# Kernel optimization log

Hardware: AMD Instinct MI355X
Metric: run time of the kernel (lower is better)

The kernel has to match this reference:

```python
import jax, jax.numpy as jnp
import numpy as np
from math import sqrt

D_MODEL = 1024
D_HEAD = 128
TAU = 30.0
B, L = 8, 2048


def setup_inputs() -> dict:
    key = jax.random.key(0)
    k1, k2, k3, k4 = jax.random.split(key, 4)
    x = jax.random.normal(k1, (B, L, D_MODEL), dtype=jnp.float32)
    attention_mask = jnp.ones((B, L), dtype=jnp.int32)
    W_Q = jax.random.normal(k2, (D_HEAD, D_MODEL), dtype=jnp.float32)
    W_K = jax.random.normal(k3, (D_HEAD, D_MODEL), dtype=jnp.float32)
    W_V = jax.random.normal(k4, (D_HEAD, D_MODEL), dtype=jnp.float32)
    return {"input": x, "attention_mask": attention_mask, "W_Q": W_Q, "W_K": W_K, "W_V": W_V}


def reference(input, attention_mask, W_Q, W_K, W_V):
    # Single-head projections: [B, L, d_head]
    Q = input @ W_Q.T
    K = input @ W_K.T
    V = input @ W_V.T
    # Scaled scores: [B, L, L]
    S = jnp.einsum("bqd,bkd->bqk", Q, K) / sqrt(D_HEAD)
    # tanh soft-capping (mode == 'tanh-clipped')
    S = TAU * jnp.tanh(S)
    l = input.shape[1]
    # causal mask: strictly upper triangle -> -inf
    causal = jnp.triu(jnp.ones((l, l), dtype=bool), k=1)
    S = jnp.where(causal[None, :, :], -jnp.inf, S)
    # padding mask on keys: [B, 1, L]
    S = jnp.where(attention_mask[:, None, :] == 0, -jnp.inf, S)
    Attn = jax.nn.softmax(S, axis=-1)
    return Attn @ V
```

## Files before the change

### kernel.cpp

```cpp
#include <hip/hip_runtime.h>
#include <hip/hip_bf16.h>

#define BATCH  8
#define SEQ    2048
#define DMODEL 1024
#define DHEAD  128

typedef __attribute__((ext_vector_type(4))) float f32x4;
typedef __attribute__((ext_vector_type(4))) float f4;
typedef _Float16 f16;
typedef __attribute__((ext_vector_type(8))) _Float16 f16x8;
typedef __attribute__((ext_vector_type(8))) __bf16 bf16x8;
typedef __attribute__((ext_vector_type(16))) unsigned short u16x16;

__device__ __forceinline__ unsigned short f2bf(float f) {
    unsigned u = __builtin_bit_cast(unsigned, f);
    u += 0x7fffu + ((u >> 16) & 1u);
    return (unsigned short)(u >> 16);
}

#if __has_builtin(__builtin_amdgcn_exp2f)
#define EXP2(x) __builtin_amdgcn_exp2f(x)
#else
#define EXP2(x) exp2f(x)
#endif

__device__ __forceinline__ float fast_rcp(float x) {
#if __has_builtin(__builtin_amdgcn_rcpf)
    return __builtin_amdgcn_rcpf(x);
#else
    return 1.0f / x;
#endif
}

__device__ __forceinline__ void async_copy16(const void* g, void* l) {
    __builtin_amdgcn_global_load_lds(
        (const __attribute__((address_space(1))) unsigned int*)g,
        (__attribute__((address_space(3))) unsigned int*)l,
        16, 0, 0);
}

__global__ __launch_bounds__(256) void wsplit_kernel(
    const float* __restrict__ WQ, const float* __restrict__ WK,
    const float* __restrict__ WV, f16* __restrict__ Wsp)
{
    const int gid = blockIdx.x * 256 + threadIdx.x;
    const int row = gid & 127;
    const int hi  = (gid >> 7) & 3;
    const int ks  = (gid >> 9) & 31;
    const int mat = gid >> 14;
    const float* W = (mat < 2) ? WQ : (mat < 4) ? WK : WV;
    const float* src = W + (size_t)row * DMODEL + ks * 32 + hi * 8;
    f4 v0 = *(const f4*)src, v1 = *(const f4*)(src + 4);
    const bool lopart = (mat == 1 || mat == 3);
    f16x8 o;
    #pragma unroll
    for (int j = 0; j < 4; ++j) {
        f16 h0 = (f16)v0[j], h1 = (f16)v1[j];
        o[j]     = lopart ? (f16)(v0[j] - (float)h0) : h0;
        o[j + 4] = lopart ? (f16)(v1[j] - (float)h1) : h1;
    }
    *reinterpret_cast<f16x8*>(Wsp + (size_t)gid * 8) = o;
}

__global__ __launch_bounds__(256) void proj_kernel(
    const float* __restrict__ x, const f16* __restrict__ Wsp,
    f16* __restrict__ Qh, f16* __restrict__ Ql,
    f16* __restrict__ Kh, f16* __restrict__ Kl,
    unsigned short* __restrict__ Vtb)
{
    __shared__ f16 Wl[2][5][4][64][8];
    __shared__ f16 Ax[2][2][4][4][17][8];

    const int tid  = threadIdx.x;
    const int lane = tid & 63;
    const int w    = tid >> 6;
    const int lo   = lane & 15;
    const int hi   = lane >> 4;
    const int m0   = blockIdx.x * 64;
    const int bn   = blockIdx.y;

    const int xrow = tid >> 2;
    const int xg   = tid & 3;
    const int xrb  = xrow >> 4, xro = xrow & 15;

    f32x4 accQ[4] = {}, accK[4] = {}, accV[4] = {};

    const float* xbase = x + (size_t)(m0 + xrow) * DMODEL + xg * 8;
    const f16*   wsrc0 = Wsp + (size_t)(w * 128 + bn * 64 + lane) * 8;

    f4 rx0, rx1;
    auto loadX = [&](int ks) {
        rx0 = *(const f4*)(xbase + ks * 32);
        rx1 = *(const f4*)(xbase + ks * 32 + 4);
    };
    auto writeX = [&](int buf) {
        f16x8 h8, l8;
        #pragma unroll
        for (int j = 0; j < 4; ++j) {
            f16 h0 = (f16)rx0[j]; h8[j]     = h0; l8[j]     = (f16)(rx0[j] - (float)h0);
            f16 h1 = (f16)rx1[j]; h8[j + 4] = h1; l8[j + 4] = (f16)(rx1[j] - (float)h1);
        }
        *reinterpret_cast<f16x8*>(&Ax[buf][0][xrb][xg][xro][0]) = h8;
        *reinterpret_cast<f16x8*>(&Ax[buf][1][xrb][xg][xro][0]) = l8;
    };
    auto stageW = [&](int ks, int buf) {
        #pragma unroll
        for (int m = 0; m < 5; ++m)
            async_copy16(wsrc0 + (size_t)(m * 32 + ks) * 4096,
                         &Wl[buf][m][w][0][0]);
    };

    stageW(0, 0);
    loadX(0);
    writeX(0);
    __syncthreads();

    for (int ks = 0; ks < 32; ++ks) {
        const int cur = ks & 1;
        if (ks < 31) { stageW(ks + 1, cur ^ 1); loadX(ks + 1); }

        f16x8 W5[5];
        #pragma unroll
        for (int m = 0; m < 5; ++m)
            W5[m] = *reinterpret_cast<const f16x8*>(&Wl[cur][m][hi][w * 16 + lo][0]);

        #pragma unroll
        for (int rb = 0; rb < 4; ++rb) {
            f16x8 ah = *reinterpret_cast<const f16x8*>(&Ax[cur][0][rb][hi][lo][0]);
            f16x8 al = *reinterpret_cast<const f16x8*>(&Ax[cur][1][rb][hi][lo][0]);
            accQ[rb] = __builtin_amdgcn_mfma_f32_16x16x32_f16(ah, W5[0], accQ[rb], 0, 0, 0);
            accQ[rb] = __builtin_amdgcn_mfma_f32_16x16x32_f16(ah, W5[1], accQ[rb], 0, 0, 0);
            accQ[rb] = __builtin_amdgcn_mfma_f32_16x16x32_f16(al, W5[0], accQ[rb], 0, 0, 0);
            accK[rb] = __builtin_amdgcn_mfma_f32_16x16x32_f16(ah, W5[2], accK[rb], 0, 0, 0);
            accK[rb] = __builtin_amdgcn_mfma_f32_16x16x32_f16(ah, W5[3], accK[rb], 0, 0, 0);
            accK[rb] = __builtin_amdgcn_mfma_f32_16x16x32_f16(al, W5[2], accK[rb], 0, 0, 0);
            accV[rb] = __builtin_amdgcn_mfma_f32_16x16x32_f16(ah, W5[4], accV[rb], 0, 0, 0);
        }
        if (ks < 31) writeX(cur ^ 1);
        __syncthreads();
    }

    #pragma unroll
    for (int rb = 0; rb < 4; ++rb)
        #pragma unroll
        for (int r = 0; r < 4; ++r) {
            const int m = m0 + rb * 16 + hi * 4 + r;
            const int n = bn * 64 + w * 16 + lo;
            const size_t idx = (size_t)m * DHEAD + n;
            float vq = accQ[rb][r];
            f16 hq = (f16)vq;
            Qh[idx] = hq; Ql[idx] = (f16)(vq - (float)hq);
            float vk = accK[rb][r];
            f16 hk = (f16)vk;
            Kh[idx] = hk; Kl[idx] = (f16)(vk - (float)hk);
            const int bb = m >> 11, l = m & 2047;
            Vtb[((size_t)bb * DHEAD + n) * SEQ + l] = f2bf(accV[rb][r]);
        }
}

#define PART_STRIDE 8256
__global__ __launch_bounds__(512) void attn_kernel(
    const f16* __restrict__ Qh, const f16* __restrict__ Ql,
    const f16* __restrict__ Kh, const f16* __restrict__ Kl,
    const unsigned short* __restrict__ Vtb, const int* __restrict__ mask,
    float* __restrict__ part)
{
    __shared__ f16 Khs[2][64][136];
    __shared__ f16 Kls[2][64][136];
    __shared__ unsigned short Vs[2][128][72];
    __shared__ int Ms[2][64];
    __shared__ unsigned short Plds[8][16][40];

    const int tid  = threadIdx.x;
    const int lane = tid & 63;
    const int w    = tid >> 6;
    const int lo   = lane & 15;
    const int hi   = lane >> 4;
    const int wq   = w & 3;
    const int wk   = w >> 2;
    const int b    = blockIdx.x;
    const int qs   = 31 - (int)blockIdx.y;
    const int z    = blockIdx.z;
    const int qrow = qs * 64 + wq * 16;

    const float c2p = 0.25506061907448296f;
    const float c1  = -86.561702453337804f;

    f16x8 qh[4], ql[4];
    {
        const size_t off = ((size_t)(b * SEQ + qrow + lo)) * DHEAD + hi * 8;
        #pragma unroll
        for (int c = 0; c < 4; ++c) {
            qh[c] = *reinterpret_cast<const f16x8*>(Qh + off + c * 32);
            ql[c] = *reinterpret_cast<const f16x8*>(Ql + off + c * 32);
        }
    }

    const int krow = tid >> 3;
    const int kcol = (tid & 7) * 16;
    const int vrow = tid >> 2;
    const int vcol = (tid & 3) * 16;

    f16x8  rKh0, rKh1, rKl0, rKl1;
    u16x16 rV;
    int    rM = 0;

    auto load_tile = [&](int kb) {
        const size_t koff = ((size_t)(b * SEQ + kb + krow)) * DHEAD + kcol;
        rKh0 = *reinterpret_cast<const f16x8*>(Kh + koff);
        rKh1 = *reinterpret_cast<const f16x8*>(Kh + koff + 8);
        rKl0 = *reinterpret_cast<const f16x8*>(Kl + koff);
        rKl1 = *reinterpret_cast<const f16x8*>(Kl + koff + 8);
        rV   = *reinterpret_cast<const u16x16*>(Vtb + ((size_t)b * DHEAD + vrow) * SEQ + kb + vcol);
        if (tid < 64) rM = mask[b * SEQ + kb + tid];
    };
    auto write_tile = [&](int buf) {
        *reinterpret_cast<f16x8*>(&Khs[buf][krow][kcol])     = rKh0;
        *reinterpret_cast<f16x8*>(&Khs[buf][krow][kcol + 8]) = rKh1;
        *reinterpret_cast<f16x8*>(&Kls[buf][krow][kcol])     = rKl0;
        *reinterpret_cast<f16x8*>(&Kls[buf][krow][kcol + 8]) = rKl1;
        *reinterpret_cast<u16x16*>(&Vs[buf][vrow][vcol]) = rV;
        if (tid < 64) Ms[buf][tid] = rM;
    };

    load_tile(z * 64);
    write_tile(0);
    __syncthreads();

    f32x4 acc[8] = {};
    float rs[4] = {0.f, 0.f, 0.f, 0.f};

    int cnt = 0;
    for (int it = z; it <= qs; it += 2, ++cnt) {
        const int cur = cnt & 1;
        const bool havenext = (it + 2 <= qs);
        if (havenext) load_tile((it + 2) * 64);

        const int kb = it * 64 + wk * 32;
        if (kb <= qrow + 15) {
            #pragma unroll
            for (int h = 0; h < 2; ++h) {
                f32x4 s = {};
                #pragma unroll
                for (int c = 0; c < 4; ++c) {
                    f16x8 fkh = *reinterpret_cast<const f16x8*>(&Khs[cur][wk * 32 + h * 16 + lo][c * 32 + hi * 8]);
                    f16x8 fkl = *reinterpret_cast<const f16x8*>(&Kls[cur][wk * 32 + h * 16 + lo][c * 32 + hi * 8]);
                    s = __builtin_amdgcn_mfma_f32_16x16x32_f16(qh[c], fkh, s, 0, 0, 0);
                    s = __builtin_amdgcn_mfma_f32_16x16x32_f16(qh[c], fkl, s, 0, 0, 0);
                    s = __builtin_amdgcn_mfma_f32_16x16x32_f16(ql[c], fkh, s, 0, 0, 0);
                }
                const int key = kb + h * 16 + lo;
                const int mk  = Ms[cur][wk * 32 + h * 16 + lo];
                #pragma unroll
                for (int r = 0; r < 4; ++r) {
                    const int q = qrow + hi * 4 + r;
                    float t = EXP2(s[r] * c2p);
                    float p = EXP2(c1 * fast_rcp(t + 1.0f));
                    p = (key <= q && mk != 0) ? p : 0.0f;
                    rs[r] += p;
                    Plds[w][hi * 4 + r][h * 16 + lo] = f2bf(p);
                }
            }
            bf16x8 pa = *reinterpret_cast<const bf16x8*>(&Plds[w][lo][hi * 8]);
            #pragma unroll
            for (int dt = 0; dt < 8; ++dt) {
                bf16x8 vf = *reinterpret_cast<const bf16x8*>(&Vs[cur][dt * 16 + lo][wk * 32 + hi * 8]);
                acc[dt] = __builtin_amdgcn_mfma_f32_16x16x32_bf16(pa, vf, acc[dt], 0, 0, 0);
            }
        }

        if (havenext) write_tile(cur ^ 1);
        __syncthreads();
    }

    float* red = (float*)&Khs[0][0][0];
    if (wk == 1) {
        float* dst = red + ((size_t)wq * 64 + lane) * 36;
        #pragma unroll
        for (int dt = 0; dt < 8; ++dt)
            #pragma unroll
            for (int r = 0; r < 4; ++r) dst[dt * 4 + r] = acc[dt][r];
        #pragma unroll
        for (int r = 0; r < 4; ++r) dst[32 + r] = rs[r];
    }
    __syncthreads();
    if (wk == 0) {
        const float* src = red + ((size_t)wq * 64 + lane) * 36;
        #pragma unroll
        for (int dt = 0; dt < 8; ++dt)
            #pragma unroll
            for (int r = 0; r < 4; ++r) acc[dt][r] += src[dt * 4 + r];
        float rsum[4];
        #pragma unroll
        for (int r = 0; r < 4; ++r) {
            float v = rs[r] + src[32 + r];
            v += __shfl_xor(v, 1);
            v += __shfl_xor(v, 2);
            v += __shfl_xor(v, 4);
            v += __shfl_xor(v, 8);
            rsum[r] = v;
        }
        float* P = part + (((size_t)b * 32 + qs) * 2 + z) * PART_STRIDE;
        #pragma unroll
        for (int dt = 0; dt < 8; ++dt)
            #pragma unroll
            for (int r = 0; r < 4; ++r)
                P[(wq * 16 + hi * 4 + r) * 128 + dt * 16 + lo] = acc[dt][r];
        if (lo == 0)
            #pragma unroll
            for (int r = 0; r < 4; ++r)
                P[8192 + wq * 16 + hi * 4 + r] = rsum[r];
    }
}

__global__ __launch_bounds__(256) void merge_kernel(
    const float* __restrict__ part, float* __restrict__ out)
{
    const int gid = blockIdx.x * 256 + threadIdx.x;
    const int col = (gid & 31) * 4;
    const int q   = gid >> 5;
    const int b   = q >> 11, l = q & 2047;
    const int qs  = l >> 6, row = l & 63;
    const float* P0 = part + (((size_t)b * 32 + qs) * 2) * PART_STRIDE;
    const float* P1 = P0 + PART_STRIDE;
    f4 a0 = *(const f4*)(P0 + row * 128 + col);
    f4 a1 = *(const f4*)(P1 + row * 128 + col);
    float inv = fast_rcp(P0[8192 + row] + P1[8192 + row]);
    f4 o;
    #pragma unroll
    for (int j = 0; j < 4; ++j) o[j] = (a0[j] + a1[j]) * inv;
    *(f4*)(out + (size_t)q * 128 + col) = o;
}

extern "C" void kernel_launch(void* const* d_in, const int* in_sizes, int n_in,
                              void* d_out, int out_size, void* d_ws, size_t ws_size,
                              hipStream_t stream) {
    const float* x   = (const float*)d_in[0];
    const int*   msk = (const int*)d_in[1];
    const float* WQ  = (const float*)d_in[2];
    const float* WK  = (const float*)d_in[3];
    const float* WV  = (const float*)d_in[4];
    float* out = (float*)d_out;

    const size_t NE = (size_t)BATCH * SEQ * DHEAD;
    f16* Qh = (f16*)d_ws;
    f16* Ql = Qh + NE;
    f16* Kh = Ql + NE;
    f16* Kl = Kh + NE;
    unsigned short* Vtb = (unsigned short*)(Kl + NE);
    f16* Wsp = (f16*)(Vtb + NE);
    float* part = (float*)(Wsp + (size_t)5 * 32 * 4096);

    wsplit_kernel<<<320, 256, 0, stream>>>(WQ, WK, WV, Wsp);
    proj_kernel<<<dim3(BATCH * SEQ / 64, 2), 256, 0, stream>>>(x, Wsp, Qh, Ql, Kh, Kl, Vtb);
    attn_kernel<<<dim3(BATCH, 32, 2), 512, 0, stream>>>(Qh, Ql, Kh, Kl, Vtb, msk, part);
    merge_kernel<<<2048, 256, 0, stream>>>(part, out);
}
```

Measured before the change: 98.89 us.

## Load projection weights directly from global and deepen x staging to 128-wide K

The projection kernel no longer stages weight fragments through LDS with async global-to-LDS copies. Each lane now reads its W fragments straight from global memory into registers. The x tile is staged 128 K-elements at a time instead of 32, so there are 8 iterations with 8 barriers instead of 32. Launch bounds now request 2 blocks per SM. The intent is to cut LDS traffic and synchronisation, at the cost of more register pressure and weight loads that depend on cache hits instead of a prefetch.

New measurement: 92.68 us. 1.07x faster.

```diff
diff --git a/kernel.cpp b/kernel.cpp
--- a/kernel.cpp
+++ b/kernel.cpp
@@ -31,13 +31,6 @@
 #else
     return 1.0f / x;
 #endif
-}
-
-__device__ __forceinline__ void async_copy16(const void* g, void* l) {
-    __builtin_amdgcn_global_load_lds(
-        (const __attribute__((address_space(1))) unsigned int*)g,
-        (__attribute__((address_space(3))) unsigned int*)l,
-        16, 0, 0);
 }
 
 __global__ __launch_bounds__(256) void wsplit_kernel(
@@ -63,14 +56,13 @@
     *reinterpret_cast<f16x8*>(Wsp + (size_t)gid * 8) = o;
 }
 
-__global__ __launch_bounds__(256) void proj_kernel(
+__global__ __launch_bounds__(256, 2) void proj_kernel(
     const float* __restrict__ x, const f16* __restrict__ Wsp,
     f16* __restrict__ Qh, f16* __restrict__ Ql,
     f16* __restrict__ Kh, f16* __restrict__ Kl,
     unsigned short* __restrict__ Vtb)
 {
-    __shared__ f16 Wl[2][5][4][64][8];
-    __shared__ f16 Ax[2][2][4][4][17][8];
+    __shared__ f16 Ax[2][2][4][16][17][8];
 
     const int tid  = threadIdx.x;
     const int lane = tid & 63;
@@ -79,6 +71,7 @@
     const int hi   = lane >> 4;
     const int m0   = blockIdx.x * 64;
     const int bn   = blockIdx.y;
+    const int fi   = hi * 128 + bn * 64 + w * 16 + lo;
 
     const int xrow = tid >> 2;
     const int xg   = tid & 3;
@@ -87,57 +80,63 @@
     f32x4 accQ[4] = {}, accK[4] = {}, accV[4] = {};
 
     const float* xbase = x + (size_t)(m0 + xrow) * DMODEL + xg * 8;
-    const f16*   wsrc0 = Wsp + (size_t)(w * 128 + bn * 64 + lane) * 8;
-
-    f4 rx0, rx1;
-    auto loadX = [&](int ks) {
-        rx0 = *(const f4*)(xbase + ks * 32);
-        rx1 = *(const f4*)(xbase + ks * 32 + 4);
+    const f16*   wbase = Wsp + (size_t)fi * 8;
+
+    f4 rx[8];
+    auto loadX = [&](int ks4) {
+        const float* p = xbase + ks4 * 128;
+        #pragma unroll
+        for (int k = 0; k < 4; ++k) {
+            rx[2 * k]     = *(const f4*)(p + k * 32);
+            rx[2 * k + 1] = *(const f4*)(p + k * 32 + 4);
+        }
+    };
+    auto cvt8 = [](f4 v0, f4 v1, f16x8& h8, f16x8& l8) {
+        #pragma unroll
+        for (int j = 0; j < 4; ++j) {
+            f16 h0 = (f16)v0[j]; h8[j]     = h0; l8[j]     = (f16)(v0[j] - (float)h0);
+            f16 h1 = (f16)v1[j]; h8[j + 4] = h1; l8[j + 4] = (f16)(v1[j] - (float)h1);
+        }
     };
     auto writeX = [&](int buf) {
-        f16x8 h8, l8;
-        #pragma unroll
-        for (int j = 0; j < 4; ++j) {
-            f16 h0 = (f16)rx0[j]; h8[j]     = h0; l8[j]     = (f16)(rx0[j] - (float)h0);
-            f16 h1 = (f16)rx1[j]; h8[j + 4] = h1; l8[j + 4] = (f16)(rx1[j] - (float)h1);
-        }
-        *reinterpret_cast<f16x8*>(&Ax[buf][0][xrb][xg][xro][0]) = h8;
-        *reinterpret_cast<f16x8*>(&Ax[buf][1][xrb][xg][xro][0]) = l8;
-    };
-    auto stageW = [&](int ks, int buf) {
-        #pragma unroll
-        for (int m = 0; m < 5; ++m)
-            async_copy16(wsrc0 + (size_t)(m * 32 + ks) * 4096,
-                         &Wl[buf][m][w][0][0]);
-    };
-
-    stageW(0, 0);
+        #pragma unroll
+        for (int k = 0; k < 4; ++k) {
+            f16x8 h8, l8;
+            cvt8(rx[2 * k], rx[2 * k + 1], h8, l8);
+            *reinterpret_cast<f16x8*>(&Ax[buf][0][xrb][xg + 4 * k][xro][0]) = h8;
+            *reinterpret_cast<f16x8*>(&Ax[buf][1][xrb][xg + 4 * k][xro][0]) = l8;
+        }
+    };
+
     loadX(0);
     writeX(0);
     __syncthreads();
 
-    for (int ks = 0; ks < 32; ++ks) {
-        const int cur = ks & 1;
-        if (ks < 31) { stageW(ks + 1, cur ^ 1); loadX(ks + 1); }
-
-        f16x8 W5[5];
-        #pragma unroll
-        for (int m = 0; m < 5; ++m)
-            W5[m] = *reinterpret_cast<const f16x8*>(&Wl[cur][m][hi][w * 16 + lo][0]);
-
-        #pragma unroll
-        for (int rb = 0; rb < 4; ++rb) {
-            f16x8 ah = *reinterpret_cast<const f16x8*>(&Ax[cur][0][rb][hi][lo][0]);
-            f16x8 al = *reinterpret_cast<const f16x8*>(&Ax[cur][1][rb][hi][lo][0]);
-            accQ[rb] = __builtin_amdgcn_mfma_f32_16x16x32_f16(ah, W5[0], accQ[rb], 0, 0, 0);
-            accQ[rb] = __builtin_amdgcn_mfma_f32_16x16x32_f16(ah, W5[1], accQ[rb], 0, 0, 0);
-            accQ[rb] = __builtin_amdgcn_mfma_f32_16x16x32_f16(al, W5[0], accQ[rb], 0, 0, 0);
-            accK[rb] = __builtin_amdgcn_mfma_f32_16x16x32_f16(ah, W5[2], accK[rb], 0, 0, 0);
-            accK[rb] = __builtin_amdgcn_mfma_f32_16x16x32_f16(ah, W5[3], accK[rb], 0, 0, 0);
-            accK[rb] = __builtin_amdgcn_mfma_f32_16x16x32_f16(al, W5[2], accK[rb], 0, 0, 0);
-            accV[rb] = __builtin_amdgcn_mfma_f32_16x16x32_f16(ah, W5[4], accV[rb], 0, 0, 0);
-        }
-        if (ks < 31) writeX(cur ^ 1);
+    for (int ks4 = 0; ks4 < 8; ++ks4) {
+        const int cur = ks4 & 1;
+        if (ks4 < 7) loadX(ks4 + 1);
+
+        #pragma unroll
+        for (int kk = 0; kk < 4; ++kk) {
+            f16x8 W5[5];
+            #pragma unroll
+            for (int m = 0; m < 5; ++m)
+                W5[m] = *reinterpret_cast<const f16x8*>(
+                    wbase + (size_t)(m * 32 + ks4 * 4 + kk) * 4096);
+            #pragma unroll
+            for (int rb = 0; rb < 4; ++rb) {
+                f16x8 ah = *reinterpret_cast<const f16x8*>(&Ax[cur][0][rb][kk * 4 + hi][lo][0]);
+                f16x8 al = *reinterpret_cast<const f16x8*>(&Ax[cur][1][rb][kk * 4 + hi][lo][0]);
+                accQ[rb] = __builtin_amdgcn_mfma_f32_16x16x32_f16(ah, W5[0], accQ[rb], 0, 0, 0);
+                accQ[rb] = __builtin_amdgcn_mfma_f32_16x16x32_f16(ah, W5[1], accQ[rb], 0, 0, 0);
+                accQ[rb] = __builtin_amdgcn_mfma_f32_16x16x32_f16(al, W5[0], accQ[rb], 0, 0, 0);
+                accK[rb] = __builtin_amdgcn_mfma_f32_16x16x32_f16(ah, W5[2], accK[rb], 0, 0, 0);
+                accK[rb] = __builtin_amdgcn_mfma_f32_16x16x32_f16(ah, W5[3], accK[rb], 0, 0, 0);
+                accK[rb] = __builtin_amdgcn_mfma_f32_16x16x32_f16(al, W5[2], accK[rb], 0, 0, 0);
+                accV[rb] = __builtin_amdgcn_mfma_f32_16x16x32_f16(ah, W5[4], accV[rb], 0, 0, 0);
+            }
+        }
+        if (ks4 < 7) writeX(cur ^ 1);
         __syncthreads();
     }
 
```
